# Performance work log

Hardware: AMD Instinct MI355X
Metric: run time of the kernel (lower is better)

The kernel has to match this reference:

```python
import jax, jax.numpy as jnp
import numpy as np

LAMBDA_TEMPORAL = 0.5
LAMBDA_IDENTITY = 0.1
EPS = 1e-6


def setup_inputs() -> dict:
    key = jax.random.key(0)
    k1, k2, k3 = jax.random.split(key, 3)
    B, T, N = 16, 256, 2048
    pred_tracks_3d = jax.random.normal(k1, (B, T, N, 3), dtype=jnp.float32)
    gt_tracks_3d = jax.random.normal(k2, (B, T, N, 3), dtype=jnp.float32)
    gt_visibility = jax.random.uniform(k3, (B, T, N), dtype=jnp.float32)
    return {
        'pred_tracks_3d': pred_tracks_3d,
        'gt_tracks_3d': gt_tracks_3d,
        'gt_visibility': gt_visibility,
    }


def _compute_losses(pred, gt, vis):
    # visibility mask (B, T, N)
    m = (vis > 0.5).astype(pred.dtype)
    num_visible = jnp.sum(m)

    coord_w = jnp.array([1.0, 1.0, 2.0], dtype=pred.dtype)
    weighted_sq = jnp.square(pred - gt) * coord_w  # (B,T,N,3)
    recon = jnp.where(
        num_visible > 0,
        jnp.sum(weighted_sq * m[..., None]) / jnp.maximum(num_visible, 1.0),
        0.0,
    )

    # --- temporal: masked velocity MSE (visible in both adjacent frames) ---
    pred_vel = pred[:, 1:] - pred[:, :-1]
    gt_vel = gt[:, 1:] - gt[:, :-1]
    vel_mask = m[:, 1:] * m[:, :-1]  # (B,T-1,N)
    num_vel = jnp.sum(vel_mask)
    temporal = jnp.where(
        num_vel > 0,
        jnp.sum(jnp.square(pred_vel - gt_vel) * vel_mask[..., None]) / jnp.maximum(num_vel, 1.0),
        0.0,
    )

    # --- identity: per-point unbiased variance ratio over visible (b,t) samples ---
    n = jnp.sum(m, axis=(0, 1))  # (N,) visible count per point

    def masked_var(x):
        # unbiased (ddof=1) per-point, per-coord variance over masked (B,T) entries
        mean = jnp.einsum('btn,btnc->nc', m, x) / jnp.maximum(n, 1.0)[:, None]
        ss = jnp.einsum('btn,btnc->nc', m, jnp.square(x - mean[None, None]))
        return ss / jnp.maximum(n - 1.0, 1.0)[:, None]  # (N,3)

    pred_var = masked_var(pred)
    gt_var = masked_var(gt)
    var_ratio = jnp.sum(jnp.abs(pred_var - gt_var), axis=1) / (jnp.sum(gt_var, axis=1) + EPS)
    num_points = pred.shape[2]
    identity = jnp.sum(jnp.where(n > 1, var_ratio, 0.0)) / num_points

    # --- adaptive re-weighting (no-grad in original) ---
    rl = jax.lax.stop_gradient(recon)
    tl = jax.lax.stop_gradient(temporal)
    il = jax.lax.stop_gradient(identity)
    all_pos = (rl > 0) & (tl > 0) & (il > 0)
    max_comp = jnp.maximum(jnp.maximum(rl, tl), il)
    target = max_comp / 3.0
    thresh = 10.0 * target

    def adjust(base, comp):
        return jnp.where(all_pos & (comp > thresh), base * target / jnp.maximum(comp, 1e-30), base)

    rec_w = adjust(1.0, rl)
    temp_w = adjust(LAMBDA_TEMPORAL, tl)
    id_w = adjust(LAMBDA_IDENTITY, il)

    total = rec_w * recon + temp_w * temporal + id_w * identity
    return jnp.stack([total, recon, temporal, identity])


def reference(pred_tracks_3d, gt_tracks_3d, gt_visibility):
    # returns [total_loss, reconstruction_loss, temporal_loss, identity_loss]
    return _compute_losses(pred_tracks_3d, gt_tracks_3d, gt_visibility)
```

## Files before the change

### kernel.cpp

```cpp
#include <hip/hip_runtime.h>

#define BB 16
#define TT 256
#define NN 2048
#define TC 16
#define NSLICE 8
#define WSBASE 16


__device__ __forceinline__ float waveReduceSum(float v) {
#pragma unroll
  for (int o = 32; o > 0; o >>= 1) v += __shfl_down(v, o, 64);
  return v;
}

__global__ __launch_bounds__(256, 8) void stats_kernel(
    const float* __restrict__ pred, const float* __restrict__ gt,
    const float* __restrict__ vis, float* __restrict__ ws) {
  const int n  = blockIdx.x * 256 + threadIdx.x;
  const int b  = blockIdx.y;
  const int t0 = blockIdx.z * TC;

  const size_t frame0 = (size_t)(b * TT + t0) * NN + n;
  const float3* __restrict__ pp = (const float3*)pred + frame0;
  const float3* __restrict__ gp = (const float3*)gt + frame0;
  const float*  __restrict__ vp = vis + frame0;

  float cnt = 0.f;
  float sp0 = 0, sp1 = 0, sp2 = 0, qp0 = 0, qp1 = 0, qp2 = 0;
  float sg0 = 0, sg1 = 0, sg2 = 0, qg0 = 0, qg1 = 0, qg2 = 0;
  float recon = 0, temporal = 0, nvel = 0;

  float3 ppv, pgv;
  float mprev;
  {
    const long off = (t0 == 0) ? 0 : -(long)NN;
    ppv = pp[off];
    pgv = gp[off];
    float v = vp[off];
    mprev = (t0 != 0 && v > 0.5f) ? 1.f : 0.f;
  }

#pragma unroll
  for (int i = 0; i < TC; ++i) {
    float3 a = pp[(size_t)i * NN];
    float3 g = gp[(size_t)i * NN];
    float v = vp[(size_t)i * NN];
    float m = (v > 0.5f) ? 1.f : 0.f;

    cnt += m;
    sp0 += m * a.x; sp1 += m * a.y; sp2 += m * a.z;
    qp0 += m * a.x * a.x; qp1 += m * a.y * a.y; qp2 += m * a.z * a.z;
    sg0 += m * g.x; sg1 += m * g.y; sg2 += m * g.z;
    qg0 += m * g.x * g.x; qg1 += m * g.y * g.y; qg2 += m * g.z * g.z;
    float d0 = a.x - g.x, d1 = a.y - g.y, d2 = a.z - g.z;
    recon += m * (d0 * d0 + d1 * d1 + 2.f * d2 * d2);

    float mv = m * mprev;
    float vx = (a.x - ppv.x) - (g.x - pgv.x);
    float vy = (a.y - ppv.y) - (g.y - pgv.y);
    float vz = (a.z - ppv.z) - (g.z - pgv.z);
    temporal += mv * (vx * vx + vy * vy + vz * vz);
    nvel += mv;

    ppv = a; pgv = g; mprev = m;
  }

  float* pts = ws + WSBASE + (size_t)(b & (NSLICE - 1)) * 13 * NN;
  atomicAdd(&pts[0 * NN + n], cnt);
  atomicAdd(&pts[1 * NN + n], sp0);
  atomicAdd(&pts[2 * NN + n], sp1);
  atomicAdd(&pts[3 * NN + n], sp2);
  atomicAdd(&pts[4 * NN + n], qp0);
  atomicAdd(&pts[5 * NN + n], qp1);
  atomicAdd(&pts[6 * NN + n], qp2);
  atomicAdd(&pts[7 * NN + n], sg0);
  atomicAdd(&pts[8 * NN + n], sg1);
  atomicAdd(&pts[9 * NN + n], sg2);
  atomicAdd(&pts[10 * NN + n], qg0);
  atomicAdd(&pts[11 * NN + n], qg1);
  atomicAdd(&pts[12 * NN + n], qg2);

  __shared__ float sred[3][4];
  float r0 = waveReduceSum(recon);
  float r1 = waveReduceSum(temporal);
  float r2 = waveReduceSum(nvel);
  int lane = threadIdx.x & 63, w = threadIdx.x >> 6;
  if (lane == 0) { sred[0][w] = r0; sred[1][w] = r1; sred[2][w] = r2; }
  __syncthreads();
  if (threadIdx.x < 3) {
    float s = sred[threadIdx.x][0] + sred[threadIdx.x][1] +
              sred[threadIdx.x][2] + sred[threadIdx.x][3];
    atomicAdd(&ws[threadIdx.x], s);
  }
}

__global__ __launch_bounds__(256) void identity_kernel(float* __restrict__ ws) {
  const int n = blockIdx.x * 256 + threadIdx.x;
  const float* base = ws + WSBASE;
  float st[13];
#pragma unroll
  for (int k = 0; k < 13; ++k) st[k] = 0.f;
#pragma unroll
  for (int s = 0; s < NSLICE; ++s) {
    const float* pts = base + (size_t)s * 13 * NN;
#pragma unroll
    for (int k = 0; k < 13; ++k) st[k] += pts[k * NN + n];
  }
  float c = st[0];
  float sp0 = st[1], sp1 = st[2], sp2 = st[3];
  float qp0 = st[4], qp1 = st[5], qp2 = st[6];
  float sg0 = st[7], sg1 = st[8], sg2 = st[9];
  float qg0 = st[10], qg1 = st[11], qg2 = st[12];

  float inv = 1.f / fmaxf(c, 1.f);
  float dv  = 1.f / fmaxf(c - 1.f, 1.f);
  float pv0 = (qp0 - sp0 * sp0 * inv) * dv;
  float pv1 = (qp1 - sp1 * sp1 * inv) * dv;
  float pv2 = (qp2 - sp2 * sp2 * inv) * dv;
  float gv0 = (qg0 - sg0 * sg0 * inv) * dv;
  float gv1 = (qg1 - sg1 * sg1 * inv) * dv;
  float gv2 = (qg2 - sg2 * sg2 * inv) * dv;

  float num = fabsf(pv0 - gv0) + fabsf(pv1 - gv1) + fabsf(pv2 - gv2);
  float den = gv0 + gv1 + gv2 + 1e-6f;
  float contrib = (c > 1.f) ? (num / den) : 0.f;

  __shared__ float sred[2][4];
  float r0 = waveReduceSum(contrib);
  float r1 = waveReduceSum(c);
  int lane = threadIdx.x & 63, w = threadIdx.x >> 6;
  if (lane == 0) { sred[0][w] = r0; sred[1][w] = r1; }
  __syncthreads();
  if (threadIdx.x < 2) {
    float s = sred[threadIdx.x][0] + sred[threadIdx.x][1] +
              sred[threadIdx.x][2] + sred[threadIdx.x][3];
    atomicAdd(&ws[3 + threadIdx.x], s);
  }
}

__global__ void finalize_kernel(const float* __restrict__ ws, float* __restrict__ out) {
  float nv = ws[4];
  float recon = (nv > 0.f) ? ws[0] / fmaxf(nv, 1.f) : 0.f;
  float nvel = ws[2];
  float temporal = (nvel > 0.f) ? ws[1] / fmaxf(nvel, 1.f) : 0.f;
  float identity = ws[3] / (float)NN;

  float rl = recon, tl = temporal, il = identity;
  bool all_pos = (rl > 0.f) && (tl > 0.f) && (il > 0.f);
  float maxc = fmaxf(rl, fmaxf(tl, il));
  float target = maxc / 3.f;
  float thresh = 10.f * target;
  float rw = (all_pos && rl > thresh) ? 1.0f * target / fmaxf(rl, 1e-30f) : 1.0f;
  float tw = (all_pos && tl > thresh) ? 0.5f * target / fmaxf(tl, 1e-30f) : 0.5f;
  float iw = (all_pos && il > thresh) ? 0.1f * target / fmaxf(il, 1e-30f) : 0.1f;

  out[0] = rw * recon + tw * temporal + iw * identity;
  out[1] = recon;
  out[2] = temporal;
  out[3] = identity;
}

extern "C" void kernel_launch(void* const* d_in, const int* in_sizes, int n_in,
                              void* d_out, int out_size, void* d_ws, size_t ws_size,
                              hipStream_t stream) {
  const float* pred = (const float*)d_in[0];
  const float* gt   = (const float*)d_in[1];
  const float* vis  = (const float*)d_in[2];
  float* out = (float*)d_out;
  float* ws  = (float*)d_ws;

  hipMemsetAsync(d_ws, 0, (WSBASE + (size_t)NSLICE * 13 * NN) * sizeof(float), stream);

  dim3 g1(NN / 256, BB, TT / TC);
  stats_kernel<<<g1, 256, 0, stream>>>(pred, gt, vis, ws);
  identity_kernel<<<dim3(NN / 256), 256, 0, stream>>>(ws);
  finalize_kernel<<<1, 1, 0, stream>>>(ws, out);
}
```

Before: 254.4 us.

## Prefetch frames via register ring, spread atomics over more slices, fuse finalize kernel

The stats kernel now preloads four frames into a small register ring and issues the next frame's loads before computing on the current one, so memory latency overlaps with arithmetic. The launch-bounds occupancy hint drops from 8 to 6 to make room for the extra registers. Per-point accumulators are spread over 16 slices keyed by batch and time chunk, and the scalar sums get per-slice slots, to reduce atomic contention. The finalize kernel is folded into the identity kernel through a last-block-done counter, which removes one launch but adds a threadfence and extra slice reads.

```diff
diff --git a/kernel.cpp b/kernel.cpp
--- a/kernel.cpp
+++ b/kernel.cpp
@@ -4,8 +4,9 @@
 #define TT 256
 #define NN 2048
 #define TC 16
-#define NSLICE 8
-#define WSBASE 16
+#define PD 4
+#define NSLICE 16
+#define WSBASE 64
 
 
 __device__ __forceinline__ float waveReduceSum(float v) {
@@ -14,7 +15,7 @@
   return v;
 }
 
-__global__ __launch_bounds__(256, 8) void stats_kernel(
+__global__ __launch_bounds__(256, 6) void stats_kernel(
     const float* __restrict__ pred, const float* __restrict__ gt,
     const float* __restrict__ vis, float* __restrict__ ws) {
   const int n  = blockIdx.x * 256 + threadIdx.x;
@@ -25,11 +26,6 @@
   const float3* __restrict__ pp = (const float3*)pred + frame0;
   const float3* __restrict__ gp = (const float3*)gt + frame0;
   const float*  __restrict__ vp = vis + frame0;
-
-  float cnt = 0.f;
-  float sp0 = 0, sp1 = 0, sp2 = 0, qp0 = 0, qp1 = 0, qp2 = 0;
-  float sg0 = 0, sg1 = 0, sg2 = 0, qg0 = 0, qg1 = 0, qg2 = 0;
-  float recon = 0, temporal = 0, nvel = 0;
 
   float3 ppv, pgv;
   float mprev;
@@ -41,11 +37,31 @@
     mprev = (t0 != 0 && v > 0.5f) ? 1.f : 0.f;
   }
 
+  float3 P[PD], G[PD];
+  float  Vv[PD];
+#pragma unroll
+  for (int d = 0; d < PD; ++d) {
+    P[d]  = pp[(size_t)d * NN];
+    G[d]  = gp[(size_t)d * NN];
+    Vv[d] = vp[(size_t)d * NN];
+  }
+
+  float cnt = 0.f;
+  float sp0 = 0, sp1 = 0, sp2 = 0, qp0 = 0, qp1 = 0, qp2 = 0;
+  float sg0 = 0, sg1 = 0, sg2 = 0, qg0 = 0, qg1 = 0, qg2 = 0;
+  float recon = 0, temporal = 0, nvel = 0;
+
 #pragma unroll
   for (int i = 0; i < TC; ++i) {
-    float3 a = pp[(size_t)i * NN];
-    float3 g = gp[(size_t)i * NN];
-    float v = vp[(size_t)i * NN];
+    const int sl = i & (PD - 1);
+    float3 a = P[sl];
+    float3 g = G[sl];
+    float  v = Vv[sl];
+    if (i + PD < TC) {
+      P[sl]  = pp[(size_t)(i + PD) * NN];
+      G[sl]  = gp[(size_t)(i + PD) * NN];
+      Vv[sl] = vp[(size_t)(i + PD) * NN];
+    }
     float m = (v > 0.5f) ? 1.f : 0.f;
 
     cnt += m;
@@ -66,7 +82,8 @@
     ppv = a; pgv = g; mprev = m;
   }
 
-  float* pts = ws + WSBASE + (size_t)(b & (NSLICE - 1)) * 13 * NN;
+  const int slice = (b + 2 * blockIdx.z) & (NSLICE - 1);
+  float* pts = ws + WSBASE + (size_t)slice * 13 * NN;
   atomicAdd(&pts[0 * NN + n], cnt);
   atomicAdd(&pts[1 * NN + n], sp0);
   atomicAdd(&pts[2 * NN + n], sp1);
@@ -91,11 +108,12 @@
   if (threadIdx.x < 3) {
     float s = sred[threadIdx.x][0] + sred[threadIdx.x][1] +
               sred[threadIdx.x][2] + sred[threadIdx.x][3];
-    atomicAdd(&ws[threadIdx.x], s);
-  }
-}
-
-__global__ __launch_bounds__(256) void identity_kernel(float* __restrict__ ws) {
+    atomicAdd(&ws[slice * 3 + threadIdx.x], s);
+  }
+}
+
+__global__ __launch_bounds__(256) void identity_kernel(float* __restrict__ ws,
+                                                       float* __restrict__ out) {
   const int n = blockIdx.x * 256 + threadIdx.x;
   const float* base = ws + WSBASE;
   float st[13];
@@ -103,9 +121,8 @@
   for (int k = 0; k < 13; ++k) st[k] = 0.f;
 #pragma unroll
   for (int s = 0; s < NSLICE; ++s) {
-    const float* pts = base + (size_t)s * 13 * NN;
-#pragma unroll
-    for (int k = 0; k < 13; ++k) st[k] += pts[k * NN + n];
+#pragma unroll
+    for (int k = 0; k < 13; ++k) st[k] += base[(size_t)(s * 13 + k) * NN + n];
   }
   float c = st[0];
   float sp0 = st[1], sp1 = st[2], sp2 = st[3];
@@ -135,30 +152,48 @@
   if (threadIdx.x < 2) {
     float s = sred[threadIdx.x][0] + sred[threadIdx.x][1] +
               sred[threadIdx.x][2] + sred[threadIdx.x][3];
-    atomicAdd(&ws[3 + threadIdx.x], s);
-  }
-}
-
-__global__ void finalize_kernel(const float* __restrict__ ws, float* __restrict__ out) {
-  float nv = ws[4];
-  float recon = (nv > 0.f) ? ws[0] / fmaxf(nv, 1.f) : 0.f;
-  float nvel = ws[2];
-  float temporal = (nvel > 0.f) ? ws[1] / fmaxf(nvel, 1.f) : 0.f;
-  float identity = ws[3] / (float)NN;
-
-  float rl = recon, tl = temporal, il = identity;
-  bool all_pos = (rl > 0.f) && (tl > 0.f) && (il > 0.f);
-  float maxc = fmaxf(rl, fmaxf(tl, il));
-  float target = maxc / 3.f;
-  float thresh = 10.f * target;
-  float rw = (all_pos && rl > thresh) ? 1.0f * target / fmaxf(rl, 1e-30f) : 1.0f;
-  float tw = (all_pos && tl > thresh) ? 0.5f * target / fmaxf(tl, 1e-30f) : 0.5f;
-  float iw = (all_pos && il > thresh) ? 0.1f * target / fmaxf(il, 1e-30f) : 0.1f;
-
-  out[0] = rw * recon + tw * temporal + iw * identity;
-  out[1] = recon;
-  out[2] = temporal;
-  out[3] = identity;
+    atomicAdd(&ws[48 + threadIdx.x], s);
+  }
+
+  __threadfence();
+  __shared__ int isLast;
+  if (threadIdx.x == 0) {
+    int old = atomicAdd((int*)(ws + 50), 1);
+    isLast = (old == (int)gridDim.x - 1) ? 1 : 0;
+  }
+  __syncthreads();
+  if (isLast && threadIdx.x < 64) {
+    float r = 0.f, t = 0.f, v = 0.f;
+    if (lane < NSLICE) {
+      r = atomicAdd(&ws[lane * 3 + 0], 0.f);
+      t = atomicAdd(&ws[lane * 3 + 1], 0.f);
+      v = atomicAdd(&ws[lane * 3 + 2], 0.f);
+    }
+    r = waveReduceSum(r);
+    t = waveReduceSum(t);
+    v = waveReduceSum(v);
+    if (lane == 0) {
+      float idsum = atomicAdd(&ws[48], 0.f);
+      float nvis  = atomicAdd(&ws[49], 0.f);
+      float recon = (nvis > 0.f) ? r / fmaxf(nvis, 1.f) : 0.f;
+      float temporal = (v > 0.f) ? t / fmaxf(v, 1.f) : 0.f;
+      float identity = idsum / (float)NN;
+
+      float rl = recon, tl = temporal, il = identity;
+      bool all_pos = (rl > 0.f) && (tl > 0.f) && (il > 0.f);
+      float maxc = fmaxf(rl, fmaxf(tl, il));
+      float target = maxc / 3.f;
+      float thresh = 10.f * target;
+      float rw = (all_pos && rl > thresh) ? 1.0f * target / fmaxf(rl, 1e-30f) : 1.0f;
+      float tw = (all_pos && tl > thresh) ? 0.5f * target / fmaxf(tl, 1e-30f) : 0.5f;
+      float iw = (all_pos && il > thresh) ? 0.1f * target / fmaxf(il, 1e-30f) : 0.1f;
+
+      out[0] = rw * recon + tw * temporal + iw * identity;
+      out[1] = recon;
+      out[2] = temporal;
+      out[3] = identity;
+    }
+  }
 }
 
 extern "C" void kernel_launch(void* const* d_in, const int* in_sizes, int n_in,
@@ -174,6 +209,5 @@
 
   dim3 g1(NN / 256, BB, TT / TC);
   stats_kernel<<<g1, 256, 0, stream>>>(pred, gt, vis, ws);
-  identity_kernel<<<dim3(NN / 256), 256, 0, stream>>>(ws);
-  finalize_kernel<<<1, 1, 0, stream>>>(ws, out);
-}
+  identity_kernel<<<dim3(NN / 256), 256, 0, stream>>>(ws, out);
+}
```

After: 256.3 us. Within noise of the previous version (+0.7%).
